# Kernel optimization log

Hardware: AMD Instinct MI355X
Metric: run time of the kernel (lower is better)

The kernel has to match this reference:

```python
import jax, jax.numpy as jnp
import numpy as np

B, D_IN, D_H = 4096, 1024, 1024


def setup_inputs() -> dict:
    key = jax.random.key(0)
    ks = jax.random.split(key, 11)
    s = 1.0 / np.sqrt(D_IN + D_H)  # torch Linear default init scale
    inp = {
        "x": jax.random.normal(ks[0], (B, D_IN), jnp.float32),
        "h": jax.random.normal(ks[1], (B, D_H), jnp.float32),
        "c": jax.random.normal(ks[2], (B, D_H), jnp.float32),
        "W_f": jax.random.uniform(ks[3], (D_IN + D_H, D_H), jnp.float32, -s, s),
        "b_f": jax.random.uniform(ks[4], (D_H,), jnp.float32, -s, s),
        "W_i": jax.random.uniform(ks[5], (D_IN + D_H, D_H), jnp.float32, -s, s),
        "b_i": jax.random.uniform(ks[6], (D_H,), jnp.float32, -s, s),
        "W_c": jax.random.uniform(ks[7], (D_IN + D_H, D_H), jnp.float32, -s, s),
        "b_c": jax.random.uniform(ks[8], (D_H,), jnp.float32, -s, s),
        "W_o": jax.random.uniform(ks[9], (D_IN + D_H, D_H), jnp.float32, -s, s),
        "b_o": jax.random.uniform(ks[10], (D_H,), jnp.float32, -s, s),
    }
    return inp


def reference(x, h, c, W_f, b_f, W_i, b_i, W_c, b_c, W_o, b_o):
    xh = jnp.concatenate([x, h], axis=1)  # [B, D_IN+D_H]
    # fuse four gate linears into one GEMM: [B, 2H] @ [2H, 4H]
    W = jnp.concatenate([W_f, W_i, W_c, W_o], axis=1)
    b = jnp.concatenate([b_f, b_i, b_c, b_o], axis=0)
    gates = xh @ W + b  # [B, 4H]
    f_g, i_g, c_g, o_g = jnp.split(gates, 4, axis=1)
    f = jax.nn.sigmoid(f_g)
    i = jax.nn.sigmoid(i_g)
    ct = jnp.tanh(c_g)
    ot = jax.nn.sigmoid(o_g)
    c_new = f * c + i * ct
    h_new = ot * jnp.tanh(c_new)
    return (h_new, (h_new, c_new))
```

## Files before the change

kernel.cpp:

```cpp
#include <hip/hip_runtime.h>
#include <hip/hip_bf16.h>
#include <cstdint>

typedef __bf16 bf16x8 __attribute__((ext_vector_type(8)));
typedef float f32x4 __attribute__((ext_vector_type(4)));

#define BROWS 4096
#define DH    1024
#define KDIM  2048
#define NT    32

__global__ __launch_bounds__(256) void k_prep(const float* __restrict__ x,
                                              const float* __restrict__ h,
                                              const float* __restrict__ Wf,
                                              const float* __restrict__ Wi,
                                              const float* __restrict__ Wc,
                                              const float* __restrict__ Wo,
                                              __hip_bfloat16* __restrict__ xh,
                                              __hip_bfloat16* __restrict__ wt) {
  __shared__ float t[64][65];
  const int tid = threadIdx.x;
  if (blockIdx.x < 4096) {
    int64_t idx = ((int64_t)blockIdx.x * 256 + tid) * 8;
    int row = (int)(idx >> 11);
    int col = (int)(idx & 2047);
    const float* src = (col < 1024) ? (x + (int64_t)row * 1024 + col)
                                    : (h + (int64_t)row * 1024 + (col - 1024));
    float4 v0 = reinterpret_cast<const float4*>(src)[0];
    float4 v1 = reinterpret_cast<const float4*>(src)[1];
    alignas(16) __hip_bfloat16 o8[8];
    o8[0] = __float2bfloat16(v0.x); o8[1] = __float2bfloat16(v0.y);
    o8[2] = __float2bfloat16(v0.z); o8[3] = __float2bfloat16(v0.w);
    o8[4] = __float2bfloat16(v1.x); o8[5] = __float2bfloat16(v1.y);
    o8[6] = __float2bfloat16(v1.z); o8[7] = __float2bfloat16(v1.w);
    *reinterpret_cast<int4*>(xh + idx) = *reinterpret_cast<const int4*>(o8);
  } else {
    const int b = blockIdx.x - 4096;
    const int g  = b & 3;
    const int jt = (b >> 2) & 15;
    const int kt = b >> 6;
    const float* W = (g == 0) ? Wf : (g == 1) ? Wi : (g == 2) ? Wc : Wo;
    const int j0 = jt << 6, k0 = kt << 6;
#pragma unroll
    for (int i = 0; i < 4; ++i) {
      int r = (tid >> 4) + (i << 4);
      int c = (tid & 15) << 2;
      float4 v = *reinterpret_cast<const float4*>(W + (int64_t)(k0 + r) * 1024 + j0 + c);
      t[r][c + 0] = v.x; t[r][c + 1] = v.y; t[r][c + 2] = v.z; t[r][c + 3] = v.w;
    }
    __syncthreads();
#pragma unroll
    for (int i = 0; i < 2; ++i) {
      int task = tid + (i << 8);
      int rr = task >> 3;
      int kc = (task & 7) << 3;
      int np = (((jt << 2) + (rr >> 4)) << 6) + (g << 4) + (rr & 15);
      alignas(16) __hip_bfloat16 o8[8];
#pragma unroll
      for (int e = 0; e < 8; ++e) o8[e] = __float2bfloat16(t[kc + e][rr]);
      *reinterpret_cast<int4*>(wt + (int64_t)np * KDIM + k0 + kc) =
          *reinterpret_cast<const int4*>(o8);
    }
  }
}

__device__ __forceinline__ void gload16(const __hip_bfloat16* g, __hip_bfloat16* l) {
  __builtin_amdgcn_global_load_lds(
      (const __attribute__((address_space(1))) void*)g,
      (__attribute__((address_space(3))) void*)l, 16, 0, 0);
}

__device__ __forceinline__ float sig_(float v) {
  return __builtin_amdgcn_rcpf(1.0f + __expf(-v));
}
__device__ __forceinline__ float tanh_(float v) {
  return fmaf(2.0f, __builtin_amdgcn_rcpf(1.0f + __expf(-2.0f * v)), -1.0f);
}

#define STAGE(P, KH, TS)                                                               \
  do {                                                                                 \
    const int64_t gko = (int64_t)(TS) * 64 + (KH) * 32;                                \
    gload16(aG + gko,                    lds + (P) * 32768 + (KH) * 8192 + wslot);     \
    gload16(aG + gko + 128 * KDIM,       lds + (P) * 32768 + (KH) * 8192 + 4096 + wslot); \
    gload16(bG + gko,                    lds + (P) * 32768 + 16384 + (KH) * 8192 + wslot); \
    gload16(bG + gko + 128 * KDIM,       lds + (P) * 32768 + 16384 + (KH) * 8192 + 4096 + wslot); \
  } while (0)

#define PHASE(P, KH, SP, SKH, TS)                                                      \
  do {                                                                                 \
    bf16x8 av[8], bv[4];                                                               \
    _Pragma("unroll")                                                                  \
    for (int mi = 0; mi < 8; ++mi)                                                     \
      av[mi] = *reinterpret_cast<const bf16x8*>(                                       \
          lds + (P) * 32768 + (KH) * 8192 + ((wmb + mi * 16 + frow) << 5) + rx);       \
    _Pragma("unroll")                                                                  \
    for (int ni = 0; ni < 4; ++ni)                                                     \
      bv[ni] = *reinterpret_cast<const bf16x8*>(                                       \
          lds + (P) * 32768 + 16384 + (KH) * 8192 + ((wnb + ni * 16 + frow) << 5) + rx); \
    STAGE(SP, SKH, TS);                                                                \
    asm volatile("s_waitcnt vmcnt(8)" ::: "memory");                                   \
    __builtin_amdgcn_s_barrier();                                                      \
    __builtin_amdgcn_s_setprio(1);                                                     \
    _Pragma("unroll")                                                                  \
    for (int mi = 0; mi < 8; ++mi)                                                     \
      _Pragma("unroll")                                                                \
      for (int ni = 0; ni < 4; ++ni)                                                   \
        acc[mi][ni] = __builtin_amdgcn_mfma_f32_16x16x32_bf16(av[mi], bv[ni],          \
                                                              acc[mi][ni], 0, 0, 0);   \
    __builtin_amdgcn_s_setprio(0);                                                     \
    __builtin_amdgcn_s_barrier();                                                      \
  } while (0)

__global__ __launch_bounds__(512, 2) void k_lstm_gemm(
    const __hip_bfloat16* __restrict__ xh, const __hip_bfloat16* __restrict__ wt,
    const float* __restrict__ cin,
    const float* __restrict__ bfp, const float* __restrict__ bip,
    const float* __restrict__ bcp, const float* __restrict__ bop,
    float* __restrict__ out) {
  __shared__ __hip_bfloat16 lds[65536];
  const int tid  = threadIdx.x;
  const int lane = tid & 63;
  const int wid  = tid >> 6;
  const int wm = wid >> 2, wn = wid & 3;
  const int wmb = wm << 7, wnb = wn << 6;

  const int bid  = blockIdx.x;
  const int flat = ((bid & 7) << 5) | (bid >> 3);
  const int m0 = (flat & 15) << 8;
  const int n0 = (flat >> 4) << 8;

  f32x4 acc[8][4] = {};

  const int wslot = wid << 9;
  const int cl = (((lane & 3) ^ ((lane >> 3) & 3)) << 3);
  const __hip_bfloat16* aG = xh + (int64_t)(m0 + (wid << 4) + (lane >> 2)) * KDIM + cl;
  const __hip_bfloat16* bG = wt + (int64_t)(n0 + (wid << 4) + (lane >> 2)) * KDIM + cl;

  const int frow = lane & 15;
  const int rx   = (((lane >> 4) ^ ((frow >> 1) & 3)) << 3);

  STAGE(0, 0, 0);
  STAGE(0, 1, 0);
  STAGE(1, 0, 1);
  asm volatile("s_waitcnt vmcnt(8)" ::: "memory");
  __builtin_amdgcn_s_barrier();

  for (int t = 0; t < NT; t += 2) {
    const int tA = t + 1;
    const int tB = (t + 2 < NT) ? t + 2 : NT - 1;
    const int tC = (t + 3 < NT) ? t + 3 : NT - 1;
    PHASE(0, 0, 1, 1, tA);
    PHASE(0, 1, 0, 0, tB);
    PHASE(1, 0, 0, 1, tB);
    PHASE(1, 1, 1, 0, tC);
  }

  const int j = (((n0 >> 6) + wn) << 4) + frow;
  const float vbf = bfp[j], vbi = bip[j], vbc = bcp[j], vbo = bop[j];
  const int q4 = (lane >> 4) << 2;
  float* outh1 = out;
  float* outh2 = out + (int64_t)BROWS * DH;
  float* outc  = out + (int64_t)2 * BROWS * DH;
#pragma unroll
  for (int mi = 0; mi < 8; ++mi) {
    const int mbase = m0 + wmb + (mi << 4) + q4;
#pragma unroll
    for (int r = 0; r < 4; ++r) {
      const int m = mbase + r;
      const int64_t idx = (int64_t)m * DH + j;
      float fg = sig_(acc[mi][0][r] + vbf);
      float ig = sig_(acc[mi][1][r] + vbi);
      float cg = tanh_(acc[mi][2][r] + vbc);
      float og = sig_(acc[mi][3][r] + vbo);
      float cn = fg * cin[idx] + ig * cg;
      float hn = og * tanh_(cn);
      outh1[idx] = hn;
      outh2[idx] = hn;
      outc[idx]  = cn;
    }
  }
}

extern "C" void kernel_launch(void* const* d_in, const int* in_sizes, int n_in,
                              void* d_out, int out_size, void* d_ws, size_t ws_size,
                              hipStream_t stream) {
  const float* x  = (const float*)d_in[0];
  const float* h  = (const float*)d_in[1];
  const float* c  = (const float*)d_in[2];
  const float* Wf = (const float*)d_in[3];
  const float* bf = (const float*)d_in[4];
  const float* Wi = (const float*)d_in[5];
  const float* bi = (const float*)d_in[6];
  const float* Wc = (const float*)d_in[7];
  const float* bc = (const float*)d_in[8];
  const float* Wo = (const float*)d_in[9];
  const float* bo = (const float*)d_in[10];
  float* out = (float*)d_out;

  __hip_bfloat16* xh = (__hip_bfloat16*)d_ws;
  __hip_bfloat16* wt = xh + (int64_t)BROWS * KDIM;

  hipLaunchKernelGGL(k_prep, dim3(6144), dim3(256), 0, stream,
                     x, h, Wf, Wi, Wc, Wo, xh, wt);
  hipLaunchKernelGGL(k_lstm_gemm, dim3(256), dim3(512), 0, stream,
                     xh, wt, c, bf, bi, bc, bo, out);
}
```

Measured before the change: 88.28 us.

## Split GEMM phases into finer half-M steps with incremental pointer staging

```diff
diff --git a/kernel.cpp b/kernel.cpp
--- a/kernel.cpp
+++ b/kernel.cpp
@@ -64,12 +64,6 @@
   }
 }
 
-__device__ __forceinline__ void gload16(const __hip_bfloat16* g, __hip_bfloat16* l) {
-  __builtin_amdgcn_global_load_lds(
-      (const __attribute__((address_space(1))) void*)g,
-      (__attribute__((address_space(3))) void*)l, 16, 0, 0);
-}
-
 __device__ __forceinline__ float sig_(float v) {
   return __builtin_amdgcn_rcpf(1.0f + __expf(-v));
 }
@@ -77,39 +71,42 @@
   return fmaf(2.0f, __builtin_amdgcn_rcpf(1.0f + __expf(-2.0f * v)), -1.0f);
 }
 
-#define STAGE(P, KH, TS)                                                               \
-  do {                                                                                 \
-    const int64_t gko = (int64_t)(TS) * 64 + (KH) * 32;                                \
-    gload16(aG + gko,                    lds + (P) * 32768 + (KH) * 8192 + wslot);     \
-    gload16(aG + gko + 128 * KDIM,       lds + (P) * 32768 + (KH) * 8192 + 4096 + wslot); \
-    gload16(bG + gko,                    lds + (P) * 32768 + 16384 + (KH) * 8192 + wslot); \
-    gload16(bG + gko + 128 * KDIM,       lds + (P) * 32768 + 16384 + (KH) * 8192 + 4096 + wslot); \
+#define GLD(PTR, LOFF)                                                           \
+  __builtin_amdgcn_global_load_lds(                                              \
+      (const __attribute__((address_space(1))) void*)(PTR),                      \
+      (__attribute__((address_space(3))) void*)(lds + (LOFF) + wslot), 16, 0, 0)
+
+#define STG(P0, P1, LBASE)                                                       \
+  do { GLD(P0, (LBASE)); GLD(P1, (LBASE) + 4096); } while (0)
+
+#define LDSA(P, KH, MI)                                                          \
+  (*reinterpret_cast<const bf16x8*>(lds + (P) * 32768 + (KH) * 8192 + abase + (MI) * 512))
+#define LDSB(P, KH, NI)                                                          \
+  (*reinterpret_cast<const bf16x8*>(lds + (P) * 32768 + (KH) * 8192 + bbase + (NI) * 512))
+
+#define VM4 asm volatile("s_waitcnt vmcnt(4)" ::: "memory")
+#define NOVM do {} while (0)
+
+#define PHASE(P, KH, MIH, STAGE_STMT, VMSTMT)                                    \
+  do {                                                                           \
+    bf16x8 av[4];                                                                \
+    if ((MIH) == 0) {                                                            \
+      _Pragma("unroll") for (int ni = 0; ni < 4; ++ni) bv[ni] = LDSB(P, KH, ni); \
+    }                                                                            \
+    _Pragma("unroll") for (int i = 0; i < 4; ++i) av[i] = LDSA(P, KH, (MIH) * 4 + i); \
+    STAGE_STMT;                                                                  \
+    VMSTMT;                                                                      \
+    __builtin_amdgcn_s_barrier();                                                \
+    __builtin_amdgcn_s_setprio(1);                                               \
+    _Pragma("unroll") for (int i = 0; i < 4; ++i)                                \
+      _Pragma("unroll") for (int ni = 0; ni < 4; ++ni)                           \
+        acc[(MIH) * 4 + i][ni] = __builtin_amdgcn_mfma_f32_16x16x32_bf16(        \
+            av[i], bv[ni], acc[(MIH) * 4 + i][ni], 0, 0, 0);                     \
+    __builtin_amdgcn_s_setprio(0);                                               \
+    __builtin_amdgcn_s_barrier();                                                \
   } while (0)
 
-#define PHASE(P, KH, SP, SKH, TS)                                                      \
-  do {                                                                                 \
-    bf16x8 av[8], bv[4];                                                               \
-    _Pragma("unroll")                                                                  \
-    for (int mi = 0; mi < 8; ++mi)                                                     \
-      av[mi] = *reinterpret_cast<const bf16x8*>(                                       \
-          lds + (P) * 32768 + (KH) * 8192 + ((wmb + mi * 16 + frow) << 5) + rx);       \
-    _Pragma("unroll")                                                                  \
-    for (int ni = 0; ni < 4; ++ni)                                                     \
-      bv[ni] = *reinterpret_cast<const bf16x8*>(                                       \
-          lds + (P) * 32768 + 16384 + (KH) * 8192 + ((wnb + ni * 16 + frow) << 5) + rx); \
-    STAGE(SP, SKH, TS);                                                                \
-    asm volatile("s_waitcnt vmcnt(8)" ::: "memory");                                   \
-    __builtin_amdgcn_s_barrier();                                                      \
-    __builtin_amdgcn_s_setprio(1);                                                     \
-    _Pragma("unroll")                                                                  \
-    for (int mi = 0; mi < 8; ++mi)                                                     \
-      _Pragma("unroll")                                                                \
-      for (int ni = 0; ni < 4; ++ni)                                                   \
-        acc[mi][ni] = __builtin_amdgcn_mfma_f32_16x16x32_bf16(av[mi], bv[ni],          \
-                                                              acc[mi][ni], 0, 0, 0);   \
-    __builtin_amdgcn_s_setprio(0);                                                     \
-    __builtin_amdgcn_s_barrier();                                                      \
-  } while (0)
+#define ADV do { a0 += 64; a1 += 64; b0 += 64; b1 += 64; } while (0)
 
 __global__ __launch_bounds__(512, 2) void k_lstm_gemm(
     const __hip_bfloat16* __restrict__ xh, const __hip_bfloat16* __restrict__ wt,
@@ -133,26 +130,41 @@
 
   const int wslot = wid << 9;
   const int cl = (((lane & 3) ^ ((lane >> 3) & 3)) << 3);
-  const __hip_bfloat16* aG = xh + (int64_t)(m0 + (wid << 4) + (lane >> 2)) * KDIM + cl;
-  const __hip_bfloat16* bG = wt + (int64_t)(n0 + (wid << 4) + (lane >> 2)) * KDIM + cl;
+  const __hip_bfloat16* a0 = xh + (int64_t)(m0 + (tid >> 2)) * KDIM + cl;
+  const __hip_bfloat16* a1 = a0 + 128 * KDIM;
+  const __hip_bfloat16* b0 = wt + (int64_t)(n0 + (tid >> 2)) * KDIM + cl;
+  const __hip_bfloat16* b1 = b0 + 128 * KDIM;
 
   const int frow = lane & 15;
   const int rx   = (((lane >> 4) ^ ((frow >> 1) & 3)) << 3);
-
-  STAGE(0, 0, 0);
-  STAGE(0, 1, 0);
-  STAGE(1, 0, 1);
-  asm volatile("s_waitcnt vmcnt(8)" ::: "memory");
+  const int abase = ((wmb + frow) << 5) + rx;
+  const int bbase = 16384 + ((wnb + frow) << 5) + rx;
+
+  STG(a0, a1, 0);
+  STG(b0, b1, 16384);
+  STG(a0 + 32, a1 + 32, 8192);
+  STG(b0 + 32, b1 + 32, 16384 + 8192);
+  ADV;
+  asm volatile("s_waitcnt vmcnt(4)" ::: "memory");
   __builtin_amdgcn_s_barrier();
 
   for (int t = 0; t < NT; t += 2) {
-    const int tA = t + 1;
-    const int tB = (t + 2 < NT) ? t + 2 : NT - 1;
-    const int tC = (t + 3 < NT) ? t + 3 : NT - 1;
-    PHASE(0, 0, 1, 1, tA);
-    PHASE(0, 1, 0, 0, tB);
-    PHASE(1, 0, 0, 1, tB);
-    PHASE(1, 1, 1, 0, tC);
+    {
+      bf16x8 bv[4];
+      PHASE(0, 0, 0, STG(a0, a1, 32768), NOVM);
+      PHASE(0, 0, 1, STG(b0, b1, 32768 + 16384), VM4);
+      PHASE(0, 1, 0, STG(a0 + 32, a1 + 32, 32768 + 8192), NOVM);
+      PHASE(0, 1, 1, STG(b0 + 32, b1 + 32, 32768 + 16384 + 8192), VM4);
+    }
+    if (t != 30) ADV;
+    {
+      bf16x8 bv[4];
+      PHASE(1, 0, 0, STG(a0, a1, 0), NOVM);
+      PHASE(1, 0, 1, STG(b0, b1, 16384), VM4);
+      PHASE(1, 1, 0, STG(a0 + 32, a1 + 32, 8192), NOVM);
+      PHASE(1, 1, 1, STG(b0 + 32, b1 + 32, 16384 + 8192), VM4);
+    }
+    ADV;
   }
 
   const int j = (((n0 >> 6) + wn) << 4) + frow;
```

After: 86.64 us. Within noise of the previous version (-1.9%).
